# Optimization experiments

Hardware: AMD Instinct MI355X
Metric: run time of the kernel (lower is better)

## Reference

```python
import jax, jax.numpy as jnp
import numpy as np

B = 4096
IN_DIM = 256
OUT_DIM = 256
COND_DIM = 128
HID = 512
HYPER_OUT = IN_DIM * OUT_DIM  # 65536


def setup_inputs() -> dict:
    key = jax.random.key(0)
    ks = jax.random.split(key, 8)

    def xavier(k, shape):
        fan_in, fan_out = shape[0], shape[1]
        std = np.sqrt(2.0 / (fan_in + fan_out))
        return jax.random.normal(k, shape, dtype=jnp.float32) * std

    return {
        "input_h": jax.random.normal(ks[0], (B, IN_DIM), dtype=jnp.float32),
        "condition_z": jax.random.normal(ks[1], (B, COND_DIM), dtype=jnp.float32),
        # hypernet: Linear(COND_DIM, HID) -> ReLU -> Linear(HID, HYPER_OUT)
        "W1": xavier(ks[2], (COND_DIM, HID)),
        "b1": jnp.zeros((HID,), dtype=jnp.float32),
        "W2": xavier(ks[3], (HID, HYPER_OUT)),
        "b2": jnp.zeros((HYPER_OUT,), dtype=jnp.float32),
        # static bias (use_bias=True, generate_bias=False)
        "bias": jnp.zeros((1, OUT_DIM), dtype=jnp.float32),
    }


def reference(input_h, condition_z, W1, b1, W2, b2, bias):
    # HyperNet MLP generates per-sample weight matrix
    hyp = jax.nn.relu(condition_z @ W1 + b1)          # [B, HID]
    weight_S = hyp @ W2 + b2                          # [B, IN*OUT]  (1 GB intermediate)
    weight_S = weight_S.reshape(-1, IN_DIM, OUT_DIM)  # [B, IN, OUT]
    # batched matmul: [B,1,IN] x [B,IN,OUT] -> [B,OUT]
    out = jnp.einsum("bi,bio->bo", input_h, weight_S)
    return out + bias
```

## Files before the change

kernel.cpp:

```cpp
#include <hip/hip_runtime.h>
#include <hip/hip_bf16.h>
#include <stdint.h>


typedef _Float16 f16x8 __attribute__((ext_vector_type(8)));
typedef _Float16 f16x2 __attribute__((ext_vector_type(2)));
typedef float    f32x4 __attribute__((ext_vector_type(4)));
typedef float    f32x16 __attribute__((ext_vector_type(16)));
typedef uint32_t u32x4 __attribute__((ext_vector_type(4)));

#define KTILES     2052
#define TILE_BYTES 32768
#define HB_OFF     (9u*1024u*1024u)
#define BP_OFF     (12u*1024u*1024u)

__global__ void k_init_out(const float* __restrict__ bias, float* __restrict__ out) {
    int idx = blockIdx.x * 256 + threadIdx.x;
    out[idx] = bias[idx & 255];
}

__global__ void k_hcast(const float* __restrict__ h, _Float16* __restrict__ hb) {
    int i = (blockIdx.x * 256 + threadIdx.x) * 8;
    f32x4 a = *(const f32x4*)(h + i);
    f32x4 b = *(const f32x4*)(h + i + 4);
    f16x8 v;
    v[0] = (_Float16)a[0]; v[1] = (_Float16)a[1]; v[2] = (_Float16)a[2]; v[3] = (_Float16)a[3];
    v[4] = (_Float16)b[0]; v[5] = (_Float16)b[1]; v[6] = (_Float16)b[2]; v[7] = (_Float16)b[3];
    *(f16x8*)(hb + i) = v;
}

__global__ void k_hypT(const float* __restrict__ z, const float* __restrict__ W1,
                       const float* __restrict__ b1, float* __restrict__ hypT) {
    int blk = blockIdx.x;
    int t   = threadIdx.x;
    __shared__ float zs[32][128];
    int b0 = blk * 32;
#pragma unroll
    for (int u = 0; u < 8; ++u) {
        int idx = u * 512 + t;
        zs[idx >> 7][idx & 127] = z[b0 * 128 + idx];
    }
    __syncthreads();
    float acc[32];
    float bk = b1[t];
#pragma unroll
    for (int b = 0; b < 32; ++b) acc[b] = bk;
    for (int c = 0; c < 128; ++c) {
        float w = W1[c * 512 + t];
#pragma unroll
        for (int b = 0; b < 32; ++b) acc[b] = fmaf(zs[b][c], w, acc[b]);
    }
    float* dst = hypT + (size_t)t * 4096 + b0;
#pragma unroll
    for (int v = 0; v < 8; ++v) {
        f32x4 o;
#pragma unroll
        for (int q = 0; q < 4; ++q) {
            float a = acc[v * 4 + q];
            o[q] = a > 0.f ? a : 0.f;
        }
        *(f32x4*)(dst + v * 4) = o;
    }
}

__global__ void k_pack(const float* __restrict__ W2, const float* __restrict__ b2,
                       _Float16* __restrict__ Bp) {
    __shared__ char tile[TILE_BYTES];
    int t   = blockIdx.x;
    int tid = threadIdx.x;
    long row0 = (long)t * 64;
    const float* src = (t < 2048) ? (W2 + row0 * 256) : (b2 + (row0 - 131072) * 256);
#pragma unroll
    for (int u = 0; u < 16; ++u) {
        int f = (u * 256 + tid) * 4;
        f32x4 v = *(const f32x4*)(src + f);
        int kk = f >> 8;
        int o0 = f & 255;
        int kb = ((kk >> 3) << 9) + ((kk & 7) << 1);
#pragma unroll
        for (int j = 0; j < 4; ++j) {
            int o = o0 + j;
            int addr = ((o >> 5) << 12) + kb + ((o & 31) << 4);
            *(_Float16*)(tile + addr) = (_Float16)v[j];
        }
    }
    __syncthreads();
    char* dst = (char*)Bp + (size_t)t * TILE_BYTES;
#pragma unroll
    for (int v = 0; v < 8; ++v) {
        int off = (v * 256 + tid) * 16;
        *(f32x4*)(dst + off) = *(const f32x4*)(tile + off);
    }
}

static __device__ __forceinline__ f16x8 scale8(f16x8 a, uint32_t s) {
    u32x4 ua = __builtin_bit_cast(u32x4, a);
    f16x2 sv = __builtin_bit_cast(f16x2, s);
    u32x4 r;
#pragma unroll
    for (int q = 0; q < 4; ++q) {
        f16x2 aq = __builtin_bit_cast(f16x2, (uint32_t)ua[q]);
        f16x2 rq = aq * sv;
        r[q] = __builtin_bit_cast(uint32_t, rq);
    }
    return __builtin_bit_cast(f16x8, r);
}

__global__ __launch_bounds__(512, 2) void k_gemm(
        const _Float16* __restrict__ hb, const float* __restrict__ hypT,
        const _Float16* __restrict__ Bp, float* __restrict__ out) {
    __shared__ char smem[163840];

    const int tid  = threadIdx.x;
    const int lane = tid & 63;
    const int wid  = tid >> 6;
    const int l31  = lane & 31;
    const int hsel = lane >> 5;
    const int colb = wid * 32 + l31;

    const int bid = blockIdx.x;
    const int s   = bid & 7;
    const int mt  = bid >> 3;
    const int k0  = s * 64;
    const int row_base = mt * 128;
    const int NT  = (s == 7) ? 260 : 256;

    uint32_t* shyp32 = (uint32_t*)(smem + 131072);

#pragma unroll
    for (int u = 0; u < 4; ++u) {
        int f  = (u * 512 + tid) * 4;
        int kk = f >> 7;
        int r  = f & 127;
        f32x4 v = *(const f32x4*)(hypT + (size_t)(k0 + kk) * 4096 + row_base + r);
#pragma unroll
        for (int q = 0; q < 4; ++q) {
            int rr = r + q;
            _Float16 hf = (_Float16)v[q];
            uint32_t d  = (uint32_t)__builtin_bit_cast(uint16_t, hf) * 0x10001u;
            shyp32[kk * 128 + (rr & 31) * 4 + (rr >> 5)] = d;
        }
    }

    auto tile_of = [&](int idx) {
        return (idx < 256) ? ((k0 + (idx & 63)) * 4 + (idx >> 6)) : (2048 + idx - 256);
    };
    auto stage = [&](int slot, int t) {
        const char* gsrc = (const char*)Bp + (size_t)t * TILE_BYTES + wid * 4096 + lane * 16;
        char* ldst = smem + slot * 32768 + wid * 4096;
#pragma unroll
        for (int q = 0; q < 4; ++q)
            __builtin_amdgcn_global_load_lds(
                (const __attribute__((address_space(1))) void*)(gsrc + q * 1024),
                (__attribute__((address_space(3))) void*)(ldst + q * 1024), 16, 0, 0);
    };

    stage(0, tile_of(0));
    stage(1, tile_of(1));
    stage(2, tile_of(2));
    __syncthreads();

    int boffs[4];
#pragma unroll
    for (int ks = 0; ks < 4; ++ks)
        boffs[ks] = wid * 4096 + ks * 1024 + hsel * 512 + l31 * 16;
    const int soff = l31 * 4;

    f32x16 acc[4];
#pragma unroll
    for (int i = 0; i < 4; ++i)
#pragma unroll
        for (int q = 0; q < 16; ++q) acc[i][q] = 0.0f;

    const u32x4 oneD = {0x3C003C00u, 0x3C003C00u, 0x3C003C00u, 0x3C003C00u};

    f16x8 bC[4], bN[4];
    u32x4 sdC, sdN;
    f16x8 af[4][4];

    {
        const char* sB = smem;
#pragma unroll
        for (int ks = 0; ks < 4; ++ks) bC[ks] = *(const f16x8*)(sB + boffs[ks]);
        sdC = *(const u32x4*)(shyp32 + soff);
    }

#define PIPE(BC, SDC_, BN, SDN_, IDX)                                                        \
  {                                                                                          \
    const int _i = (IDX);                                                                    \
    if (_i + 3 < NT) stage((_i + 3) & 3, tile_of(_i + 3));                                   \
    if (_i + 1 < NT) {                                                                       \
      int _stg  = (_i + 3 < NT) ? _i + 3 : NT - 1;                                           \
      int _pend = _stg - (_i + 1);                                                           \
      if (_pend >= 2)      asm volatile("s_waitcnt vmcnt(8)" ::: "memory");                  \
      else if (_pend == 1) asm volatile("s_waitcnt vmcnt(4)" ::: "memory");                  \
      else                 asm volatile("s_waitcnt vmcnt(0)" ::: "memory");                  \
      const char* _sB = smem + ((_i + 1) & 3) * 32768;                                       \
      _Pragma("unroll")                                                                      \
      for (int ks = 0; ks < 4; ++ks) BN[ks] = *(const f16x8*)(_sB + boffs[ks]);              \
      SDN_ = (_i + 1 < 256) ? *(const u32x4*)(shyp32 + ((_i + 1) & 63) * 128 + soff) : oneD; \
    }                                                                                        \
    __builtin_amdgcn_s_setprio(1);                                                           \
    _Pragma("unroll")                                                                        \
    for (int m = 0; m < 4; ++m) {                                                            \
      uint32_t _sd = SDC_[m];                                                                \
      _Pragma("unroll")                                                                      \
      for (int ks = 0; ks < 4; ++ks)                                                         \
        acc[m] = __builtin_amdgcn_mfma_f32_32x32x16_f16(scale8(af[m][ks], _sd), BC[ks],      \
                                                        acc[m], 0, 0, 0);                    \
    }                                                                                        \
    __builtin_amdgcn_s_setprio(0);                                                           \
  }

    for (int G = 0; G < 4; ++G) {
#pragma unroll
        for (int m = 0; m < 4; ++m)
#pragma unroll
            for (int ks = 0; ks < 4; ++ks)
                af[m][ks] = *(const f16x8*)(hb + (size_t)(row_base + m * 32 + l31) * 256
                                            + G * 64 + ks * 16 + hsel * 8);

        for (int jj = 0; jj < 64; jj += 2) {
            const int idx = G * 64 + jj;
            PIPE(bC, sdC, bN, sdN, idx);
            PIPE(bN, sdN, bC, sdC, idx + 1);
        }
    }

    if (s == 7) {
        for (int g = 0; g < 4; ++g) {
            int idx = 256 + g;
            if (idx + 3 < 260) stage((idx + 3) & 3, tile_of(idx + 3));
#pragma unroll
            for (int m = 0; m < 4; ++m)
#pragma unroll
                for (int ks = 0; ks < 4; ++ks)
                    af[m][ks] = *(const f16x8*)(hb + (size_t)(row_base + m * 32 + l31) * 256
                                                + g * 64 + ks * 16 + hsel * 8);
            asm volatile("s_waitcnt vmcnt(0)" ::: "memory");
            const char* sB = smem + (idx & 3) * 32768;
            f16x8 tB[4];
#pragma unroll
            for (int ks = 0; ks < 4; ++ks) tB[ks] = *(const f16x8*)(sB + boffs[ks]);
#pragma unroll
            for (int m = 0; m < 4; ++m)
#pragma unroll
                for (int ks = 0; ks < 4; ++ks)
                    acc[m] = __builtin_amdgcn_mfma_f32_32x32x16_f16(af[m][ks], tB[ks],
                                                                    acc[m], 0, 0, 0);
        }
    }

#pragma unroll
    for (int m = 0; m < 4; ++m)
#pragma unroll
        for (int reg = 0; reg < 16; ++reg) {
            int row = row_base + m * 32 + hsel * 4 + (reg & 3) + 8 * (reg >> 2);
            atomicAdd(&out[row * 256 + colb], acc[m][reg]);
        }
}

extern "C" void kernel_launch(void* const* d_in, const int* in_sizes, int n_in,
                              void* d_out, int out_size, void* d_ws, size_t ws_size,
                              hipStream_t stream) {
    const float* h    = (const float*)d_in[0];
    const float* z    = (const float*)d_in[1];
    const float* W1   = (const float*)d_in[2];
    const float* b1   = (const float*)d_in[3];
    const float* W2   = (const float*)d_in[4];
    const float* b2   = (const float*)d_in[5];
    const float* bias = (const float*)d_in[6];
    float* out = (float*)d_out;

    float*     hypT = (float*)d_ws;
    _Float16*  hb   = (_Float16*)((char*)d_ws + HB_OFF);
    _Float16*  Bp   = (_Float16*)((char*)d_ws + BP_OFF);

    k_pack    <<<KTILES, 256, 0, stream>>>(W2, b2, Bp);
    k_hypT    <<<128,    512, 0, stream>>>(z, W1, b1, hypT);
    k_hcast   <<<512,    256, 0, stream>>>(h, hb);
    k_init_out<<<4096,   256, 0, stream>>>(bias, out);
    k_gemm    <<<256,    512, 0, stream>>>(hb, hypT, Bp, out);
}
```

Before: 334.5 us.

## Halve GEMM M-tile to 64 rows and double-buffer LDS for more blocks

The GEMM block's row tile drops from 128 to 64, so the grid doubles from 256 to 512 blocks and each block holds half the accumulators. The LDS B-tile ring goes from four slots with three in flight to two slots with one in flight. Shared memory per block falls to 80 KB and launch bounds ask for 4 blocks per CU. The aim is to fill all CUs (256 blocks leave many idle on a large GPU) and raise occupancy. The cost is that each B tile is now read from global memory twice as often, with less reuse per load and a shallower prefetch pipeline.

```diff
diff --git a/kernel.cpp b/kernel.cpp
--- a/kernel.cpp
+++ b/kernel.cpp
@@ -7,6 +7,7 @@
 typedef _Float16 f16x2 __attribute__((ext_vector_type(2)));
 typedef float    f32x4 __attribute__((ext_vector_type(4)));
 typedef float    f32x16 __attribute__((ext_vector_type(16)));
+typedef uint32_t u32x2 __attribute__((ext_vector_type(2)));
 typedef uint32_t u32x4 __attribute__((ext_vector_type(4)));
 
 #define KTILES     2052
@@ -106,10 +107,10 @@
     return __builtin_bit_cast(f16x8, r);
 }
 
-__global__ __launch_bounds__(512, 2) void k_gemm(
+__global__ __launch_bounds__(512, 4) void k_gemm(
         const _Float16* __restrict__ hb, const float* __restrict__ hypT,
         const _Float16* __restrict__ Bp, float* __restrict__ out) {
-    __shared__ char smem[163840];
+    __shared__ char smem[81920];
 
     const int tid  = threadIdx.x;
     const int lane = tid & 63;
@@ -122,23 +123,23 @@
     const int s   = bid & 7;
     const int mt  = bid >> 3;
     const int k0  = s * 64;
-    const int row_base = mt * 128;
+    const int row_base = mt * 64;
     const int NT  = (s == 7) ? 260 : 256;
 
-    uint32_t* shyp32 = (uint32_t*)(smem + 131072);
-
-#pragma unroll
-    for (int u = 0; u < 4; ++u) {
-        int f  = (u * 512 + tid) * 4;
-        int kk = f >> 7;
-        int r  = f & 127;
-        f32x4 v = *(const f32x4*)(hypT + (size_t)(k0 + kk) * 4096 + row_base + r);
-#pragma unroll
-        for (int q = 0; q < 4; ++q) {
-            int rr = r + q;
-            _Float16 hf = (_Float16)v[q];
+    uint32_t* shyp32 = (uint32_t*)(smem + 65536);
+
+    {
+        int kk = tid >> 3;
+        int r0 = (tid & 7) * 8;
+        const float* hp = hypT + (size_t)(k0 + kk) * 4096 + row_base + r0;
+        f32x4 v0 = *(const f32x4*)hp;
+        f32x4 v1 = *(const f32x4*)(hp + 4);
+#pragma unroll
+        for (int q = 0; q < 8; ++q) {
+            int r = r0 + q;
+            _Float16 hf = (_Float16)((q < 4) ? v0[q] : v1[q - 4]);
             uint32_t d  = (uint32_t)__builtin_bit_cast(uint16_t, hf) * 0x10001u;
-            shyp32[kk * 128 + (rr & 31) * 4 + (rr >> 5)] = d;
+            shyp32[kk * 64 + (r & 31) * 2 + (r >> 5)] = d;
         }
     }
 
@@ -157,64 +158,59 @@
 
     stage(0, tile_of(0));
     stage(1, tile_of(1));
-    stage(2, tile_of(2));
     __syncthreads();
 
     int boffs[4];
 #pragma unroll
     for (int ks = 0; ks < 4; ++ks)
         boffs[ks] = wid * 4096 + ks * 1024 + hsel * 512 + l31 * 16;
-    const int soff = l31 * 4;
-
-    f32x16 acc[4];
-#pragma unroll
-    for (int i = 0; i < 4; ++i)
+    const int soff = l31 * 2;
+
+    f32x16 acc[2];
+#pragma unroll
+    for (int i = 0; i < 2; ++i)
 #pragma unroll
         for (int q = 0; q < 16; ++q) acc[i][q] = 0.0f;
 
-    const u32x4 oneD = {0x3C003C00u, 0x3C003C00u, 0x3C003C00u, 0x3C003C00u};
+    const u32x2 oneD = {0x3C003C00u, 0x3C003C00u};
 
     f16x8 bC[4], bN[4];
-    u32x4 sdC, sdN;
-    f16x8 af[4][4];
+    u32x2 sdC, sdN;
+    f16x8 af[2][4];
 
     {
-        const char* sB = smem;
-#pragma unroll
-        for (int ks = 0; ks < 4; ++ks) bC[ks] = *(const f16x8*)(sB + boffs[ks]);
-        sdC = *(const u32x4*)(shyp32 + soff);
-    }
-
-#define PIPE(BC, SDC_, BN, SDN_, IDX)                                                        \
-  {                                                                                          \
-    const int _i = (IDX);                                                                    \
-    if (_i + 3 < NT) stage((_i + 3) & 3, tile_of(_i + 3));                                   \
-    if (_i + 1 < NT) {                                                                       \
-      int _stg  = (_i + 3 < NT) ? _i + 3 : NT - 1;                                           \
-      int _pend = _stg - (_i + 1);                                                           \
-      if (_pend >= 2)      asm volatile("s_waitcnt vmcnt(8)" ::: "memory");                  \
-      else if (_pend == 1) asm volatile("s_waitcnt vmcnt(4)" ::: "memory");                  \
-      else                 asm volatile("s_waitcnt vmcnt(0)" ::: "memory");                  \
-      const char* _sB = smem + ((_i + 1) & 3) * 32768;                                       \
-      _Pragma("unroll")                                                                      \
-      for (int ks = 0; ks < 4; ++ks) BN[ks] = *(const f16x8*)(_sB + boffs[ks]);              \
-      SDN_ = (_i + 1 < 256) ? *(const u32x4*)(shyp32 + ((_i + 1) & 63) * 128 + soff) : oneD; \
-    }                                                                                        \
-    __builtin_amdgcn_s_setprio(1);                                                           \
-    _Pragma("unroll")                                                                        \
-    for (int m = 0; m < 4; ++m) {                                                            \
-      uint32_t _sd = SDC_[m];                                                                \
-      _Pragma("unroll")                                                                      \
-      for (int ks = 0; ks < 4; ++ks)                                                         \
-        acc[m] = __builtin_amdgcn_mfma_f32_32x32x16_f16(scale8(af[m][ks], _sd), BC[ks],      \
-                                                        acc[m], 0, 0, 0);                    \
-    }                                                                                        \
-    __builtin_amdgcn_s_setprio(0);                                                           \
+#pragma unroll
+        for (int ks = 0; ks < 4; ++ks) bC[ks] = *(const f16x8*)(smem + boffs[ks]);
+        sdC = *(const u32x2*)(shyp32 + soff);
+    }
+
+#define PIPE(BC, SDC_, BN, SDN_, IDX)                                                       \
+  {                                                                                         \
+    const int _i = (IDX);                                                                   \
+    if (_i + 2 < NT) stage(_i & 1, tile_of(_i + 2));                                        \
+    if (_i + 1 < NT) {                                                                      \
+      if (_i + 2 < NT) asm volatile("s_waitcnt vmcnt(4)" ::: "memory");                     \
+      else             asm volatile("s_waitcnt vmcnt(0)" ::: "memory");                     \
+      const char* _sB = smem + ((_i + 1) & 1) * 32768;                                      \
+      _Pragma("unroll")                                                                     \
+      for (int ks = 0; ks < 4; ++ks) BN[ks] = *(const f16x8*)(_sB + boffs[ks]);             \
+      SDN_ = (_i + 1 < 256) ? *(const u32x2*)(shyp32 + ((_i + 1) & 63) * 64 + soff) : oneD; \
+    }                                                                                       \
+    __builtin_amdgcn_s_setprio(1);                                                          \
+    _Pragma("unroll")                                                                       \
+    for (int m = 0; m < 2; ++m) {                                                           \
+      uint32_t _sd = SDC_[m];                                                               \
+      _Pragma("unroll")                                                                     \
+      for (int ks = 0; ks < 4; ++ks)                                                        \
+        acc[m] = __builtin_amdgcn_mfma_f32_32x32x16_f16(scale8(af[m][ks], _sd), BC[ks],     \
+                                                        acc[m], 0, 0, 0);                   \
+    }                                                                                       \
+    __builtin_amdgcn_s_setprio(0);                                                          \
   }
 
     for (int G = 0; G < 4; ++G) {
 #pragma unroll
-        for (int m = 0; m < 4; ++m)
+        for (int m = 0; m < 2; ++m)
 #pragma unroll
             for (int ks = 0; ks < 4; ++ks)
                 af[m][ks] = *(const f16x8*)(hb + (size_t)(row_base + m * 32 + l31) * 256
@@ -228,31 +224,32 @@
     }
 
     if (s == 7) {
+        asm volatile("s_waitcnt vmcnt(0)" ::: "memory");
         for (int g = 0; g < 4; ++g) {
             int idx = 256 + g;
-            if (idx + 3 < 260) stage((idx + 3) & 3, tile_of(idx + 3));
-#pragma unroll
-            for (int m = 0; m < 4; ++m)
+            const char* sB = smem + (idx & 1) * 32768;
+            f16x8 tB[4];
+#pragma unroll
+            for (int ks = 0; ks < 4; ++ks) tB[ks] = *(const f16x8*)(sB + boffs[ks]);
+            if (idx + 2 < 260) stage(idx & 1, tile_of(idx + 2));
+#pragma unroll
+            for (int m = 0; m < 2; ++m)
 #pragma unroll
                 for (int ks = 0; ks < 4; ++ks)
                     af[m][ks] = *(const f16x8*)(hb + (size_t)(row_base + m * 32 + l31) * 256
                                                 + g * 64 + ks * 16 + hsel * 8);
-            asm volatile("s_waitcnt vmcnt(0)" ::: "memory");
-            const char* sB = smem + (idx & 3) * 32768;
-            f16x8 tB[4];
-#pragma unroll
-            for (int ks = 0; ks < 4; ++ks) tB[ks] = *(const f16x8*)(sB + boffs[ks]);
-#pragma unroll
-            for (int m = 0; m < 4; ++m)
+#pragma unroll
+            for (int m = 0; m < 2; ++m)
 #pragma unroll
                 for (int ks = 0; ks < 4; ++ks)
                     acc[m] = __builtin_amdgcn_mfma_f32_32x32x16_f16(af[m][ks], tB[ks],
                                                                     acc[m], 0, 0, 0);
-        }
-    }
-
-#pragma unroll
-    for (int m = 0; m < 4; ++m)
+            asm volatile("s_waitcnt vmcnt(0)" ::: "memory");
+        }
+    }
+
+#pragma unroll
+    for (int m = 0; m < 2; ++m)
 #pragma unroll
         for (int reg = 0; reg < 16; ++reg) {
             int row = row_base + m * 32 + hsel * 4 + (reg & 3) + 8 * (reg >> 2);
@@ -280,5 +277,5 @@
     k_hypT    <<<128,    512, 0, stream>>>(z, W1, b1, hypT);
     k_hcast   <<<512,    256, 0, stream>>>(h, hb);
     k_init_out<<<4096,   256, 0, stream>>>(bias, out);
-    k_gemm    <<<256,    512, 0, stream>>>(hb, hypT, Bp, out);
-}
+    k_gemm    <<<512,    512, 0, stream>>>(hb, hypT, Bp, out);
+}
```

Measured after the change: 383.5 us. +14.7%, slower.
